# Kernel optimization log

Measured on AMD Instinct MI355X. Metric: run time of the kernel, lower is better.

Reference implementation:

```python
import jax, jax.numpy as jnp
import numpy as np

D_MODEL = 1280
NUM_HEADS = 16
GROUPS = 5
D_K = D_MODEL // NUM_HEADS  # 80
B, S = 4, 1024


def setup_inputs() -> dict:
    key = jax.random.key(0)
    ks = jax.random.split(key, 12)
    lim_dk = 1.0 / np.sqrt(D_K)
    lim_dm = 1.0 / np.sqrt(D_MODEL)
    return {
        "src": jax.random.normal(ks[0], (B, S, D_MODEL), jnp.float32),
        "k": jax.random.normal(ks[1], (B, S, D_MODEL), jnp.float32),
        "v": jax.random.normal(ks[2], (B, S, D_MODEL), jnp.float32),
        # per-head Linear(d_k, d_k) stacked: weight [H, d_k(out), d_k(in)], bias [H, d_k]
        "Wq": jax.random.uniform(ks[3], (NUM_HEADS, D_K, D_K), jnp.float32, -lim_dk, lim_dk),
        "bq": jax.random.uniform(ks[4], (NUM_HEADS, D_K), jnp.float32, -lim_dk, lim_dk),
        "Wk": jax.random.uniform(ks[5], (NUM_HEADS, D_K, D_K), jnp.float32, -lim_dk, lim_dk),
        "bk": jax.random.uniform(ks[6], (NUM_HEADS, D_K), jnp.float32, -lim_dk, lim_dk),
        "Wv": jax.random.uniform(ks[7], (NUM_HEADS, D_K, D_K), jnp.float32, -lim_dk, lim_dk),
        "bv": jax.random.uniform(ks[8], (NUM_HEADS, D_K), jnp.float32, -lim_dk, lim_dk),
        # output Linear(d_model, d_model)
        "Wo": jax.random.uniform(ks[9], (D_MODEL, D_MODEL), jnp.float32, -lim_dm, lim_dm),
        "bo": jax.random.uniform(ks[10], (D_MODEL,), jnp.float32, -lim_dm, lim_dm),
    }


def reference(src, k, v, Wq, bq, Wk, bk, Wv, bv, Wo, bo):
    # NOTE: original module ignores k, v args; q/k/v all derived from src.
    b, s, d = src.shape
    cpg = d // GROUPS
    # channel shuffle: [B,S,G,C] -> [B,S,C,G] -> [B,S,D]
    x = src.reshape(b, s, GROUPS, cpg).swapaxes(-1, -2).reshape(b, s, d)
    # split heads: [B, H, S, d_k]
    xh = x.reshape(b, s, NUM_HEADS, D_K).transpose(0, 2, 1, 3)
    # per-head distinct linears, batched over heads (torch Linear: x @ W.T + b)
    q = jnp.einsum("bhsd,hed->bhse", xh, Wq) + bq[None, :, None, :]
    kk = jnp.einsum("bhsd,hed->bhse", xh, Wk) + bk[None, :, None, :]
    vv = jnp.einsum("bhsd,hed->bhse", xh, Wv) + bv[None, :, None, :]
    scores = jnp.einsum("bhqd,bhkd->bhqk", q, kk) / jnp.sqrt(jnp.float32(D_K))
    p = jax.nn.softmax(scores, axis=-1)
    heads = jnp.einsum("bhqk,bhkd->bhqd", p, vv)
    concat = heads.transpose(0, 2, 1, 3).reshape(b, s, d)
    return concat @ Wo.T + bo
```

## Files before the change

### kernel.cpp

```cpp
#include <hip/hip_runtime.h>
#include <hip/hip_bf16.h>

#define D_MODEL 1280
#define NUM_HEADS 16
#define D_K 80
#define DP 96
#define SEQ 1024
#define BATCH 4
#define BH (BATCH*NUM_HEADS)

typedef __hip_bfloat16 bf16;
typedef short short8 __attribute__((ext_vector_type(8)));
typedef short short4v __attribute__((ext_vector_type(4)));
typedef float f32x4 __attribute__((ext_vector_type(4)));

__device__ __forceinline__ float b2f(bf16 x) { return __bfloat162float(x); }
__device__ __forceinline__ bf16 f2b(float x) { return __float2bfloat16(x); }
__device__ __forceinline__ short bbits(float x) {
    union { bf16 b; short s; } u; u.b = __float2bfloat16(x); return u.s;
}

#define MFMA16(a, b, c) __builtin_amdgcn_mfma_f32_16x16x32_bf16(a, b, c, 0, 0, 0)

__global__ __launch_bounds__(256) void cvt_all_kernel(
    const float* __restrict__ Wq, const float* __restrict__ Wk,
    const float* __restrict__ Wv, bf16* __restrict__ Wcat,
    const float* __restrict__ Wo, bf16* __restrict__ Wb)
{
    if (blockIdx.x < 1440) {
        int idx = blockIdx.x * 256 + threadIdx.x;
        int col = idx % 96;
        int row = (idx / 96) % 240;
        int h   = idx / (96 * 240);
        int mat = row / 80, e = row % 80;
        const float* W = (mat == 0) ? Wq : (mat == 1) ? Wk : Wv;
        float v = (col < 80) ? W[(size_t)(h * 80 + e) * 80 + col] : 0.f;
        Wcat[idx] = f2b(v);
    } else {
        int idx = ((blockIdx.x - 1440) * 256 + threadIdx.x) * 4;
        float4 v = *(const float4*)(Wo + idx);
        Wb[idx]     = f2b(v.x);
        Wb[idx + 1] = f2b(v.y);
        Wb[idx + 2] = f2b(v.z);
        Wb[idx + 3] = f2b(v.w);
    }
}

__global__ __launch_bounds__(256) void qkv_kernel(
    const float* __restrict__ src,
    const float* __restrict__ bq, const float* __restrict__ bk,
    const float* __restrict__ bv, const bf16* __restrict__ Wcat,
    bf16* __restrict__ Qb, bf16* __restrict__ Kb, bf16* __restrict__ Vg)
{
    __shared__ bf16 Xs[128 * 104];
    const int h = blockIdx.y;
    const int b = blockIdx.x >> 3;
    const int s0 = (blockIdx.x & 7) * 128;
    const int tid = threadIdx.x;
    const int wave = tid >> 6, lane = tid & 63;
    const int lquad = lane >> 4, lcol = lane & 15;
    const int bh = b * NUM_HEADS + h;

    #pragma unroll
    for (int it = 0; it < 10; it++) {
        int idx = tid + it * 256;
        int i = idx / 20, rem = idx % 20, c = rem >> 2, q4 = rem & 3;
        float4 v = *(const float4*)(src + (size_t)(b * SEQ + s0 + i) * D_MODEL
                                    + c * 256 + h * 16 + q4 * 4);
        bf16* x = Xs + i * 104 + c;
        x[(q4 * 4 + 0) * 5] = f2b(v.x);
        x[(q4 * 4 + 1) * 5] = f2b(v.y);
        x[(q4 * 4 + 2) * 5] = f2b(v.z);
        x[(q4 * 4 + 3) * 5] = f2b(v.w);
    }
    {
        int i = tid >> 1, half = tid & 1;
        *(uint4*)(Xs + i * 104 + 80 + half * 8) = make_uint4(0, 0, 0, 0);
    }
    __syncthreads();

    short8 xf[2][3];
    #pragma unroll
    for (int mt = 0; mt < 2; mt++)
        #pragma unroll
        for (int ks = 0; ks < 3; ks++)
            xf[mt][ks] = *(const short8*)(Xs + (wave*32 + mt*16 + lcol)*104 + ks*32 + lquad*8);

    const bf16* Wh = Wcat + (size_t)h * 240 * 96;
    const float qscale = 1.4426950408889634f * 0.11180339887498949f;

    #pragma unroll
    for (int mat = 0; mat < 2; mat++) {
        const bf16* Wm = Wh + mat * 80 * 96;
        short8 wf[5][3];
        #pragma unroll
        for (int n = 0; n < 5; n++)
            #pragma unroll
            for (int ks = 0; ks < 3; ks++)
                wf[n][ks] = *(const short8*)(Wm + (n*16 + lcol)*96 + ks*32 + lquad*8);

        f32x4 acc[2][5];
        #pragma unroll
        for (int mt = 0; mt < 2; mt++)
            #pragma unroll
            for (int n = 0; n < 5; n++)
                #pragma unroll
                for (int r = 0; r < 4; r++) acc[mt][n][r] = 0.f;

        #pragma unroll
        for (int ks = 0; ks < 3; ks++)
            #pragma unroll
            for (int n = 0; n < 5; n++) {
                acc[0][n] = MFMA16(xf[0][ks], wf[n][ks], acc[0][n]);
                acc[1][n] = MFMA16(xf[1][ks], wf[n][ks], acc[1][n]);
            }

        const float* bias = (mat == 0) ? bq : bk;
        bf16* Out = (mat == 0) ? Qb : Kb;
        const float scale = (mat == 0) ? qscale : 1.f;
        #pragma unroll
        for (int n = 0; n < 5; n++) {
            float bb = bias[h * 80 + n * 16 + lcol];
            #pragma unroll
            for (int mt = 0; mt < 2; mt++)
                #pragma unroll
                for (int r = 0; r < 4; r++) {
                    int srow = s0 + wave*32 + mt*16 + lquad*4 + r;
                    Out[((size_t)bh * SEQ + srow) * DP + n*16 + lcol] =
                        f2b((acc[mt][n][r] + bb) * scale);
                }
        }
    }
    {
        int i = tid >> 1, half = tid & 1;
        size_t row = ((size_t)bh * SEQ + s0 + i) * DP + 80 + half * 8;
        *(uint4*)(Qb + row) = make_uint4(0, 0, 0, 0);
        *(uint4*)(Kb + row) = make_uint4(0, 0, 0, 0);
    }

    {
        const bf16* Wm = Wh + 2 * 80 * 96;
        short8 wf[5][3];
        #pragma unroll
        for (int m = 0; m < 5; m++)
            #pragma unroll
            for (int ks = 0; ks < 3; ks++)
                wf[m][ks] = *(const short8*)(Wm + (m*16 + lcol)*96 + ks*32 + lquad*8);

        f32x4 acc[5][2];
        #pragma unroll
        for (int m = 0; m < 5; m++)
            #pragma unroll
            for (int nt = 0; nt < 2; nt++)
                #pragma unroll
                for (int r = 0; r < 4; r++) acc[m][nt][r] = 0.f;

        #pragma unroll
        for (int ks = 0; ks < 3; ks++)
            #pragma unroll
            for (int m = 0; m < 5; m++) {
                acc[m][0] = MFMA16(wf[m][ks], xf[0][ks], acc[m][0]);
                acc[m][1] = MFMA16(wf[m][ks], xf[1][ks], acc[m][1]);
            }

        #pragma unroll
        for (int m = 0; m < 5; m++) {
            float4 bb4 = *(const float4*)(bv + h * 80 + m * 16 + lquad * 4);
            float bb[4] = {bb4.x, bb4.y, bb4.z, bb4.w};
            #pragma unroll
            for (int nt = 0; nt < 2; nt++)
                #pragma unroll
                for (int r = 0; r < 4; r++) {
                    int e = m*16 + lquad*4 + r;
                    int token = s0 + wave*32 + nt*16 + lcol;
                    Vg[((size_t)bh * D_K + e) * SEQ + token] =
                        f2b(acc[m][nt][r] + bb[r]);
                }
        }
    }
}

__global__ __launch_bounds__(256, 2) void attn_kernel(
    const bf16* __restrict__ Qb, const bf16* __restrict__ Kb,
    const bf16* __restrict__ Vg, bf16* __restrict__ Cc)
{
    __shared__ char smem[45056];
    const int tid = threadIdx.x;
    const int wave = tid >> 6, lane = tid & 63;
    const int lquad = lane >> 4, lcol = lane & 15;
    const int bh = blockIdx.x;
    const int b = bh >> 4, h = bh & 15;
    const int q0 = blockIdx.y * 128;

    int koff[3];
    #pragma unroll
    for (int i = 0; i < 3; i++) {
        int idx = tid + i * 256;
        koff[i] = (idx / 12) * 104 + (idx % 12) * 8;
    }

    short8 qf[2][3];
    #pragma unroll
    for (int nt = 0; nt < 2; nt++)
        #pragma unroll
        for (int ks = 0; ks < 3; ks++)
            qf[nt][ks] = *(const short8*)(
                Qb + ((size_t)bh * SEQ + q0 + wave*32 + nt*16 + lcol) * DP
                   + ks*32 + lquad*8);

    uint4 kr[3];
    {
        const uint4* kg = (const uint4*)(Kb + (size_t)bh * SEQ * DP);
        #pragma unroll
        for (int i = 0; i < 3; i++) kr[i] = kg[tid + i * 256];
    }
    {
        bf16* Ks0 = (bf16*)(smem + 18432);
        #pragma unroll
        for (int i = 0; i < 3; i++) *(uint4*)(Ks0 + koff[i]) = kr[i];
    }
    __syncthreads();

    const bf16* Vrow[5];
    #pragma unroll
    for (int ne = 0; ne < 5; ne++)
        Vrow[ne] = Vg + ((size_t)bh * D_K + ne*16 + lcol) * SEQ + lquad*8;

    f32x4 Oacc[2][5];
    #pragma unroll
    for (int mt = 0; mt < 2; mt++)
        #pragma unroll
        for (int ne = 0; ne < 5; ne++)
            #pragma unroll
            for (int r = 0; r < 4; r++) Oacc[mt][ne][r] = 0.f;

    f32x4 lsum4[2];
    #pragma unroll
    for (int nt = 0; nt < 2; nt++)
        #pragma unroll
        for (int r = 0; r < 4; r++) lsum4[nt][r] = 0.f;

    bf16* Pw = (bf16*)(smem + wave * 4608);
    const f32x4 fzero = {0.f, 0.f, 0.f, 0.f};

    for (int kt = 0; kt < 16; kt++) {
        const bf16* Ksc = (const bf16*)(smem + 18432 + (kt & 1) * 13312);

        short8 vf[2][5];
        #pragma unroll
        for (int js = 0; js < 2; js++)
            #pragma unroll
            for (int ne = 0; ne < 5; ne++)
                vf[js][ne] = *(const short8*)(Vrow[ne] + kt*64 + js*32);

        if (kt < 15) {
            const uint4* kg = (const uint4*)(
                Kb + ((size_t)bh * SEQ + (kt + 1) * 64) * DP);
            #pragma unroll
            for (int i = 0; i < 3; i++) kr[i] = kg[tid + i * 256];
        }

        f32x4 st[4][2];
        __builtin_amdgcn_s_setprio(1);
        #pragma unroll
        for (int mt = 0; mt < 4; mt++) {
            short8 af = *(const short8*)(Ksc + (mt*16 + lcol)*104 + lquad*8);
            st[mt][0] = MFMA16(af, qf[0][0], fzero);
            st[mt][1] = MFMA16(af, qf[1][0], fzero);
        }
        #pragma unroll
        for (int ks = 1; ks < 3; ks++)
            #pragma unroll
            for (int mt = 0; mt < 4; mt++) {
                short8 af = *(const short8*)(Ksc + (mt*16 + lcol)*104 + ks*32 + lquad*8);
                st[mt][0] = MFMA16(af, qf[0][ks], st[mt][0]);
                st[mt][1] = MFMA16(af, qf[1][ks], st[mt][1]);
            }
        __builtin_amdgcn_s_setprio(0);

        #pragma unroll
        for (int nt = 0; nt < 2; nt++)
            #pragma unroll
            for (int mt = 0; mt < 4; mt++) {
                short4v pk;
                #pragma unroll
                for (int r = 0; r < 4; r++) {
                    float p = __builtin_amdgcn_exp2f(st[mt][nt][r]);
                    lsum4[nt][r] += p;
                    pk[r] = bbits(p);
                }
                *(short4v*)(Pw + (nt*16 + lcol)*72 + mt*16 + lquad*4) = pk;
            }

        __builtin_amdgcn_s_setprio(1);
        #pragma unroll
        for (int js = 0; js < 2; js++) {
            short8 pf0 = *(const short8*)(Pw + lcol*72 + js*32 + lquad*8);
            short8 pf1 = *(const short8*)(Pw + (16 + lcol)*72 + js*32 + lquad*8);
            #pragma unroll
            for (int ne = 0; ne < 5; ne++) {
                Oacc[0][ne] = MFMA16(pf0, vf[js][ne], Oacc[0][ne]);
                Oacc[1][ne] = MFMA16(pf1, vf[js][ne], Oacc[1][ne]);
            }
        }
        __builtin_amdgcn_s_setprio(0);

        if (kt < 15) {
            bf16* Ksn = (bf16*)(smem + 18432 + ((kt + 1) & 1) * 13312);
            #pragma unroll
            for (int i = 0; i < 3; i++) *(uint4*)(Ksn + koff[i]) = kr[i];
            __syncthreads();
        }
    }

    float inv[2];
    #pragma unroll
    for (int nt = 0; nt < 2; nt++) {
        float s = (lsum4[nt][0] + lsum4[nt][1]) + (lsum4[nt][2] + lsum4[nt][3]);
        s += __shfl_xor(s, 16);
        s += __shfl_xor(s, 32);
        inv[nt] = 1.f / s;
    }
    #pragma unroll
    for (int mt = 0; mt < 2; mt++) {
        f32x4 li;
        #pragma unroll
        for (int r = 0; r < 4; r++)
            li[r] = __shfl(inv[mt], (lane & 48) | (lquad*4 + r));
        #pragma unroll
        for (int ne = 0; ne < 5; ne++)
            #pragma unroll
            for (int r = 0; r < 4; r++) {
                int s_row = q0 + wave*32 + mt*16 + lquad*4 + r;
                int e = ne*16 + lcol;
                Cc[(size_t)(b * SEQ + s_row) * D_MODEL + h * D_K + e] =
                    f2b(Oacc[mt][ne][r] * li[r]);
            }
    }
}

__global__ __launch_bounds__(256) void proj_kernel(
    const bf16* __restrict__ Cc, const bf16* __restrict__ Wb,
    const float* __restrict__ bo, float* __restrict__ out)
{
    __shared__ bf16 As[128 * 72];
    __shared__ bf16 Bs[128 * 72];
    const int tid = threadIdx.x;
    const int wave = tid >> 6, lane = tid & 63;
    const int lquad = lane >> 4, lcol = lane & 15;
    const int t0 = blockIdx.x * 128, o0 = blockIdx.y * 128;
    const int mrow = (wave & 1) * 64, ncol = (wave >> 1) * 64;

    f32x4 acc[4][4];
    #pragma unroll
    for (int mt = 0; mt < 4; mt++)
        #pragma unroll
        for (int nt = 0; nt < 4; nt++)
            #pragma unroll
            for (int r = 0; r < 4; r++) acc[mt][nt][r] = 0.f;

    for (int kc = 0; kc < 20; kc++) {
        __syncthreads();
        #pragma unroll
        for (int i = 0; i < 4; i++) {
            int idx = tid + i * 256;
            int r = idx >> 3, c = idx & 7;
            *(uint4*)(As + r * 72 + c * 8) =
                *(const uint4*)(Cc + (size_t)(t0 + r) * D_MODEL + kc * 64 + c * 8);
            *(uint4*)(Bs + r * 72 + c * 8) =
                *(const uint4*)(Wb + (size_t)(o0 + r) * D_MODEL + kc * 64 + c * 8);
        }
        __syncthreads();
        #pragma unroll
        for (int ks = 0; ks < 2; ks++) {
            short8 am[4], bn[4];
            #pragma unroll
            for (int t = 0; t < 4; t++) {
                am[t] = *(const short8*)(As + (mrow + t*16 + lcol)*72 + ks*32 + lquad*8);
                bn[t] = *(const short8*)(Bs + (ncol + t*16 + lcol)*72 + ks*32 + lquad*8);
            }
            #pragma unroll
            for (int mt = 0; mt < 4; mt++)
                #pragma unroll
                for (int nt = 0; nt < 4; nt++)
                    acc[mt][nt] = MFMA16(am[mt], bn[nt], acc[mt][nt]);
        }
    }

    #pragma unroll
    for (int nt = 0; nt < 4; nt++) {
        float bias = bo[o0 + ncol + nt*16 + lcol];
        #pragma unroll
        for (int mt = 0; mt < 4; mt++)
            #pragma unroll
            for (int r = 0; r < 4; r++)
                out[(size_t)(t0 + mrow + mt*16 + lquad*4 + r) * D_MODEL
                    + o0 + ncol + nt*16 + lcol] = acc[mt][nt][r] + bias;
    }
}

extern "C" void kernel_launch(void* const* d_in, const int* in_sizes, int n_in,
                              void* d_out, int out_size, void* d_ws, size_t ws_size,
                              hipStream_t stream) {
    const float* src = (const float*)d_in[0];
    const float* Wq = (const float*)d_in[3];
    const float* bq = (const float*)d_in[4];
    const float* Wk = (const float*)d_in[5];
    const float* bk = (const float*)d_in[6];
    const float* Wv = (const float*)d_in[7];
    const float* bv = (const float*)d_in[8];
    const float* Wo = (const float*)d_in[9];
    const float* bo = (const float*)d_in[10];
    float* out = (float*)d_out;

    char* ws = (char*)d_ws;
    bf16* Qb = (bf16*)(ws);
    bf16* Kb = (bf16*)(ws + (size_t)12582912);
    bf16* Vg = (bf16*)(ws + (size_t)25165824);
    bf16* Cc = (bf16*)(ws + (size_t)35651584);
    bf16* Wcat = (bf16*)(ws + (size_t)35651584);
    bf16* Wb = (bf16*)(ws + (size_t)46137344);

    cvt_all_kernel<<<dim3(3040), 256, 0, stream>>>(Wq, Wk, Wv, Wcat, Wo, Wb);
    qkv_kernel<<<dim3(BATCH * SEQ / 128, NUM_HEADS), 256, 0, stream>>>(
        src, bq, bk, bv, Wcat, Qb, Kb, Vg);
    attn_kernel<<<dim3(BH, SEQ / 128), 256, 0, stream>>>(Qb, Kb, Vg, Cc);
    proj_kernel<<<dim3(SEQ * BATCH / 128, D_MODEL / 128), 256, 0, stream>>>(
        Cc, Wb, bo, out);
}
```

Measured before the change: 204.6 us.

## Stage V through LDS and halve attention block to 64 queries

The attention kernel now uses 128-thread blocks, each handling 64 queries, so the grid doubles to 1024 blocks. V tiles are loaded coalesced into shared memory and read from there, replacing per-lane global fragment loads. Q is staged through shared memory once at the start. K now uses a single buffer guarded by two barriers per iteration instead of double buffering. The aim is more parallelism and cheaper V access. The cost is twice the K/V global traffic per query and extra synchronisation each step.

Result: slower. 264.3 us (+29.1%).

```diff
diff --git a/kernel.cpp b/kernel.cpp
--- a/kernel.cpp
+++ b/kernel.cpp
@@ -180,51 +180,65 @@
     }
 }
 
-__global__ __launch_bounds__(256, 2) void attn_kernel(
+__global__ __launch_bounds__(128, 2) void attn_kernel(
     const bf16* __restrict__ Qb, const bf16* __restrict__ Kb,
     const bf16* __restrict__ Vg, bf16* __restrict__ Cc)
 {
-    __shared__ char smem[45056];
+    __shared__ char smem[38144];
+    bf16* Qs = (bf16*)smem;
+    bf16* Ks = (bf16*)(smem + 13312);
+    bf16* Vt = (bf16*)(smem + 26624);
+
     const int tid = threadIdx.x;
     const int wave = tid >> 6, lane = tid & 63;
     const int lquad = lane >> 4, lcol = lane & 15;
     const int bh = blockIdx.x;
     const int b = bh >> 4, h = bh & 15;
-    const int q0 = blockIdx.y * 128;
-
-    int koff[3];
-    #pragma unroll
-    for (int i = 0; i < 3; i++) {
-        int idx = tid + i * 256;
+    const int q0 = blockIdx.y * 64;
+
+    int koff[6], voff[5];
+    const bf16* Vbase[5];
+    #pragma unroll
+    for (int i = 0; i < 6; i++) {
+        int idx = tid + i * 128;
         koff[i] = (idx / 12) * 104 + (idx % 12) * 8;
     }
+    #pragma unroll
+    for (int i = 0; i < 5; i++) {
+        int idx = tid + i * 128;
+        voff[i] = (idx >> 3) * 72 + (idx & 7) * 8;
+        Vbase[i] = Vg + ((size_t)bh * D_K + (idx >> 3)) * SEQ + (idx & 7) * 8;
+    }
+    const uint4* Kg = (const uint4*)(Kb + (size_t)bh * SEQ * DP);
+
+    uint4 kr[6], vr[5];
+    #pragma unroll
+    for (int i = 0; i < 6; i++) kr[i] = Kg[tid + i * 128];
+    #pragma unroll
+    for (int i = 0; i < 5; i++) vr[i] = *(const uint4*)(Vbase[i]);
+
+    {
+        const uint4* qg = (const uint4*)(Qb + ((size_t)bh * SEQ + q0) * DP);
+        #pragma unroll
+        for (int i = 0; i < 6; i++) {
+            int idx = tid + i * 128, r = idx / 12, c = idx % 12;
+            *(uint4*)(Qs + r * 104 + c * 8) = qg[idx];
+        }
+    }
+    __syncthreads();
 
     short8 qf[2][3];
     #pragma unroll
     for (int nt = 0; nt < 2; nt++)
         #pragma unroll
         for (int ks = 0; ks < 3; ks++)
-            qf[nt][ks] = *(const short8*)(
-                Qb + ((size_t)bh * SEQ + q0 + wave*32 + nt*16 + lcol) * DP
-                   + ks*32 + lquad*8);
-
-    uint4 kr[3];
-    {
-        const uint4* kg = (const uint4*)(Kb + (size_t)bh * SEQ * DP);
-        #pragma unroll
-        for (int i = 0; i < 3; i++) kr[i] = kg[tid + i * 256];
-    }
-    {
-        bf16* Ks0 = (bf16*)(smem + 18432);
-        #pragma unroll
-        for (int i = 0; i < 3; i++) *(uint4*)(Ks0 + koff[i]) = kr[i];
-    }
+            qf[nt][ks] = *(const short8*)(Qs + (wave*32 + nt*16 + lcol)*104 + ks*32 + lquad*8);
+
+    #pragma unroll
+    for (int i = 0; i < 6; i++) *(uint4*)(Ks + koff[i]) = kr[i];
+    #pragma unroll
+    for (int i = 0; i < 5; i++) *(uint4*)(Vt + voff[i]) = vr[i];
     __syncthreads();
-
-    const bf16* Vrow[5];
-    #pragma unroll
-    for (int ne = 0; ne < 5; ne++)
-        Vrow[ne] = Vg + ((size_t)bh * D_K + ne*16 + lcol) * SEQ + lquad*8;
 
     f32x4 Oacc[2][5];
     #pragma unroll
@@ -244,27 +258,20 @@
     const f32x4 fzero = {0.f, 0.f, 0.f, 0.f};
 
     for (int kt = 0; kt < 16; kt++) {
-        const bf16* Ksc = (const bf16*)(smem + 18432 + (kt & 1) * 13312);
-
-        short8 vf[2][5];
-        #pragma unroll
-        for (int js = 0; js < 2; js++)
-            #pragma unroll
-            for (int ne = 0; ne < 5; ne++)
-                vf[js][ne] = *(const short8*)(Vrow[ne] + kt*64 + js*32);
-
         if (kt < 15) {
-            const uint4* kg = (const uint4*)(
-                Kb + ((size_t)bh * SEQ + (kt + 1) * 64) * DP);
-            #pragma unroll
-            for (int i = 0; i < 3; i++) kr[i] = kg[tid + i * 256];
+            const uint4* kg = Kg + (size_t)(kt + 1) * 768;
+            #pragma unroll
+            for (int i = 0; i < 6; i++) kr[i] = kg[tid + i * 128];
+            #pragma unroll
+            for (int i = 0; i < 5; i++)
+                vr[i] = *(const uint4*)(Vbase[i] + (kt + 1) * 64);
         }
 
         f32x4 st[4][2];
         __builtin_amdgcn_s_setprio(1);
         #pragma unroll
         for (int mt = 0; mt < 4; mt++) {
-            short8 af = *(const short8*)(Ksc + (mt*16 + lcol)*104 + lquad*8);
+            short8 af = *(const short8*)(Ks + (mt*16 + lcol)*104 + lquad*8);
             st[mt][0] = MFMA16(af, qf[0][0], fzero);
             st[mt][1] = MFMA16(af, qf[1][0], fzero);
         }
@@ -272,7 +279,7 @@
         for (int ks = 1; ks < 3; ks++)
             #pragma unroll
             for (int mt = 0; mt < 4; mt++) {
-                short8 af = *(const short8*)(Ksc + (mt*16 + lcol)*104 + ks*32 + lquad*8);
+                short8 af = *(const short8*)(Ks + (mt*16 + lcol)*104 + ks*32 + lquad*8);
                 st[mt][0] = MFMA16(af, qf[0][ks], st[mt][0]);
                 st[mt][1] = MFMA16(af, qf[1][ks], st[mt][1]);
             }
@@ -299,16 +306,19 @@
             short8 pf1 = *(const short8*)(Pw + (16 + lcol)*72 + js*32 + lquad*8);
             #pragma unroll
             for (int ne = 0; ne < 5; ne++) {
-                Oacc[0][ne] = MFMA16(pf0, vf[js][ne], Oacc[0][ne]);
-                Oacc[1][ne] = MFMA16(pf1, vf[js][ne], Oacc[1][ne]);
+                short8 vfx = *(const short8*)(Vt + (ne*16 + lcol)*72 + js*32 + lquad*8);
+                Oacc[0][ne] = MFMA16(pf0, vfx, Oacc[0][ne]);
+                Oacc[1][ne] = MFMA16(pf1, vfx, Oacc[1][ne]);
             }
         }
         __builtin_amdgcn_s_setprio(0);
 
         if (kt < 15) {
-            bf16* Ksn = (bf16*)(smem + 18432 + ((kt + 1) & 1) * 13312);
-            #pragma unroll
-            for (int i = 0; i < 3; i++) *(uint4*)(Ksn + koff[i]) = kr[i];
+            __syncthreads();
+            #pragma unroll
+            for (int i = 0; i < 6; i++) *(uint4*)(Ks + koff[i]) = kr[i];
+            #pragma unroll
+            for (int i = 0; i < 5; i++) *(uint4*)(Vt + voff[i]) = vr[i];
             __syncthreads();
         }
     }
@@ -424,7 +434,7 @@
     cvt_all_kernel<<<dim3(3040), 256, 0, stream>>>(Wq, Wk, Wv, Wcat, Wo, Wb);
     qkv_kernel<<<dim3(BATCH * SEQ / 128, NUM_HEADS), 256, 0, stream>>>(
         src, bq, bk, bv, Wcat, Qb, Kb, Vg);
-    attn_kernel<<<dim3(BH, SEQ / 128), 256, 0, stream>>>(Qb, Kb, Vg, Cc);
+    attn_kernel<<<dim3(BH, SEQ / 64), 128, 0, stream>>>(Qb, Kb, Vg, Cc);
     proj_kernel<<<dim3(SEQ * BATCH / 128, D_MODEL / 128), 256, 0, stream>>>(
         Cc, Wb, bo, out);
 }
```
